# Optimization experiments

Hardware: AMD Instinct MI355X
Metric: run time of the kernel (lower is better)

## Reference

```python
import jax, jax.numpy as jnp
import numpy as np
from jax import lax

KERNEL = 15
IGNORE = 255


def setup_inputs() -> dict:
    key = jax.random.key(0)
    k1, k2 = jax.random.split(key)
    B, C, H, W = 32, 2, 480, 864
    logits = jax.random.normal(k1, (B, C, H, W), dtype=jnp.float32)
    labels = jax.random.randint(k2, (B, H, W), 0, 2, dtype=jnp.int32)
    return {"logits": logits, "labels": labels}


def _boundary_edgemap(labels):
    # labels: [B, H, W] int32 with values in {0, 1, IGNORE}
    lbl = labels.astype(jnp.int32)
    # np_label = label*255, with ignore pixels set to 0 (matches cv2 path)
    np_label = jnp.where(lbl == IGNORE, 0, lbl * 255)
    win = (1, KERNEL, KERNEL)
    strides = (1, 1, 1)
    # cv2.erode with ones kernel == 15x15 min filter (border value +inf -> pad 255)
    erosion = lax.reduce_window(np_label, jnp.int32(255), lax.min, win, strides, "SAME")
    # cv2.dilate == 15x15 max filter (border value -inf -> pad 0)
    dilation = lax.reduce_window(np_label, jnp.int32(0), lax.max, win, strides, "SAME")
    boundary = dilation - erosion  # >0 exactly on the morphological boundary band
    edgemap = jnp.where(boundary > 0, lbl, IGNORE)
    edgemap = jnp.where(lbl == IGNORE, IGNORE, edgemap)
    return edgemap


def reference(logits, labels):
    # logits: [B, C, H, W] log-probabilities, labels: [B, H, W]
    edgemap = _boundary_edgemap(labels)  # [B, H, W]
    valid = edgemap != IGNORE
    tgt = jnp.where(valid, edgemap, 0)  # safe index for ignored pixels
    # gather logits[b, tgt, h, w] -> [B, H, W]
    picked = jnp.take_along_axis(logits, tgt[:, None, :, :], axis=1)[:, 0]
    # NLLLoss with ignore_index: mean of -logp over valid pixels
    n_valid = jnp.maximum(jnp.sum(valid), 1)
    loss = -jnp.sum(jnp.where(valid, picked, 0.0)) / n_valid.astype(logits.dtype)
    return loss
```

## Files before the change

### kernel.cpp

```cpp
#include <hip/hip_runtime.h>


namespace {
constexpr int B_ = 32;
constexpr int H_ = 480;
constexpr int W_ = 864;
constexpr int HW = H_ * W_;
constexpr int R_ = 7;
constexpr int TH_ = 16;
constexpr int LH = TH_ + 2 * R_;
constexpr int SW = 216;
constexpr int NSX = W_ / SW;
constexpr int NSY = H_ / TH_;
constexpr int NBLK = B_ * NSX * NSY;
}

typedef unsigned long long u64;

__device__ __forceinline__ u64 shfl_up64(u64 x, int d) {
  return __shfl_up(x, d, 64);
}
__device__ __forceinline__ u64 shfl_dn64(u64 x, int d) {
  return __shfl_down(x, d, 64);
}

extern "C" __global__ __launch_bounds__(64, 2)
void boundary_loss_main(const float* __restrict__ logits,
                        const int* __restrict__ labels,
                        double2* __restrict__ partials)
{
  const int lane = threadIdx.x;
  const int bid = blockIdx.x;
  const int lb = (bid & 7) * (NBLK / 8) + (bid >> 3);
  const int img = lb / (NSX * NSY);
  const int r = lb - img * (NSX * NSY);
  const int strip = r / NSY;
  const int seg = r - strip * NSY;
  const int gr0 = seg * TH_;

  const int cb0 = strip * SW - 8 + 4 * lane;
  const bool colinb = (cb0 >= 0) && (cb0 + 3 < W_);
  const int cbc = colinb ? cb0 : (cb0 < 0 ? 0 : W_ - 4);
  const bool labok = colinb && (lane < 58);
  const bool outl = (lane >= 2) && (lane < 56);

  const int* __restrict__ lab = labels + img * HW + cbc;
  const float* __restrict__ lg = logits + (size_t)(2 * img) * HW;
  const float* pg = lg + (size_t)gr0 * W_ + cb0;

  u64 f0 = 0, f1 = 0, f2 = 0, f3 = 0;
  unsigned cp0 = 0, cp1 = 0, cp2 = 0, cp3 = 0;
#pragma unroll
  for (int a = 0; a < LH; ++a) {
    int gr = gr0 - R_ + a;
    gr = gr < 0 ? 0 : (gr >= H_ ? H_ - 1 : gr);
    const int4 v = *(const int4*)(lab + gr * W_);
    const unsigned e1x = (v.x == 1), e1y = (v.y == 1),
                   e1z = (v.z == 1), e1w = (v.w == 1);
    f0 |= (u64)(1u + e1x) << (2 * a);
    f1 |= (u64)(1u + e1y) << (2 * a);
    f2 |= (u64)(1u + e1z) << (2 * a);
    f3 |= (u64)(1u + e1w) << (2 * a);
    if (a >= R_ && a < R_ + TH_) {
      const int sh = 2 * (a - R_);
      cp0 |= (e1x | ((unsigned)(v.x == 255) << 1)) << sh;
      cp1 |= (e1y | ((unsigned)(v.y == 255) << 1)) << sh;
      cp2 |= (e1z | ((unsigned)(v.z == 255) << 1)) << sh;
      cp3 |= (e1w | ((unsigned)(v.w == 255) << 1)) << sh;
    }
  }
  {
    const int tv = gr0 == 0 ? R_ : 0;
    const int hi = LH < (H_ + R_ - gr0) ? LH : (H_ + R_ - gr0);
    u64 rm = (2 * (hi - tv) >= 32)
                 ? ((((1ull << (2 * (hi - tv) - 32)) - 1ull) << 32) | 0xFFFFFFFFull)
                 : ((1ull << (2 * (hi - tv))) - 1ull);
    rm <<= 2 * tv;
    if (!colinb) rm = 0;
    f0 &= rm; f1 &= rm; f2 &= rm; f3 &= rm;
  }

  float4 qa0[4], qa1[4], qb0[4], qb1[4];
#define ISSUE(G0, G1, q)                                                    \
  if (outl) {                                                               \
    const float* p_ = pg + (size_t)(4 * (q)) * W_;                          \
    _Pragma("unroll") for (int o = 0; o < 4; ++o) {                         \
      G0[o] = *(const float4*)(p_ + (size_t)o * W_);                        \
      G1[o] = *(const float4*)(p_ + (size_t)o * W_ + HW);                   \
    }                                                                       \
  }

  ISSUE(qa0, qa1, 0)

  const u64 allf = f0 | f1 | f2 | f3;
  const u64 s2 = f2 | f3, s3 = f1 | s2;
  const u64 p2 = f0 | f1, p3 = p2 | f2;
  const u64 core = shfl_up64(allf, 1) | allf | shfl_dn64(allf, 1);
  u64 w0 = core | shfl_up64(s3, 2);
  u64 w1 = core | shfl_up64(s2, 2) | shfl_dn64(f0, 2);
  u64 w2 = core | shfl_up64(f3, 2) | shfl_dn64(p2, 2);
  u64 w3 = core | shfl_dn64(p3, 2);

  w0 |= w0 >> 2;  w0 |= w0 >> 4;  w0 |= w0 >> 8;  w0 |= w0 >> 14;
  w1 |= w1 >> 2;  w1 |= w1 >> 4;  w1 |= w1 >> 8;  w1 |= w1 >> 14;
  w2 |= w2 >> 2;  w2 |= w2 >> 4;  w2 |= w2 >> 8;  w2 |= w2 >> 14;
  w3 |= w3 >> 2;  w3 |= w3 >> 4;  w3 |= w3 >> 8;  w3 |= w3 >> 14;

  double lsum = 0.0;
  unsigned lcnt = 0;
#define CONSUME(G0, G1, q)                                                  \
  if (outl) {                                                               \
    _Pragma("unroll") for (int o = 0; o < 4; ++o) {                         \
      const int ro = 4 * (q) + o;                                           \
      const unsigned b0 = (unsigned)(w0 >> (2 * ro)) & 3u;                  \
      const unsigned b1 = (unsigned)(w1 >> (2 * ro)) & 3u;                  \
      const unsigned b2 = (unsigned)(w2 >> (2 * ro)) & 3u;                  \
      const unsigned b3 = (unsigned)(w3 >> (2 * ro)) & 3u;                  \
      const unsigned q0 = (cp0 >> (2 * ro)) & 3u;                           \
      const unsigned q1 = (cp1 >> (2 * ro)) & 3u;                           \
      const unsigned q2 = (cp2 >> (2 * ro)) & 3u;                           \
      const unsigned q3 = (cp3 >> (2 * ro)) & 3u;                           \
      const float4 a = G0[o], c = G1[o];                                    \
      const bool k0 = (b0 == 3u) && !(q0 & 2u);                             \
      const bool k1 = (b1 == 3u) && !(q1 & 2u);                             \
      const bool k2 = (b2 == 3u) && !(q2 & 2u);                             \
      const bool k3 = (b3 == 3u) && !(q3 & 2u);                             \
      lsum += k0 ? (double)((q0 & 1u) ? c.x : a.x) : 0.0;                   \
      lsum += k1 ? (double)((q1 & 1u) ? c.y : a.y) : 0.0;                   \
      lsum += k2 ? (double)((q2 & 1u) ? c.z : a.z) : 0.0;                   \
      lsum += k3 ? (double)((q3 & 1u) ? c.w : a.w) : 0.0;                   \
      lcnt += (unsigned)k0 + k1 + k2 + k3;                                  \
    }                                                                       \
  }

  ISSUE(qb0, qb1, 1)
  CONSUME(qa0, qa1, 0)
  __builtin_amdgcn_sched_barrier(0);
  ISSUE(qa0, qa1, 2)
  CONSUME(qb0, qb1, 1)
  __builtin_amdgcn_sched_barrier(0);
  ISSUE(qb0, qb1, 3)
  CONSUME(qa0, qa1, 2)
  __builtin_amdgcn_sched_barrier(0);
  CONSUME(qb0, qb1, 3)
#undef ISSUE
#undef CONSUME

#pragma unroll
  for (int off = 32; off > 0; off >>= 1) {
    lsum += __shfl_down(lsum, off, 64);
    lcnt += __shfl_down(lcnt, off, 64);
  }
  if (lane == 0) partials[bid] = make_double2(lsum, (double)lcnt);
}

extern "C" __global__ __launch_bounds__(1024)
void boundary_loss_final(const double2* __restrict__ partials,
                         float* __restrict__ out)
{
  __shared__ double red_s[16];
  __shared__ double red_c[16];
  const int tid = threadIdx.x;
  double s = 0.0, c = 0.0;
  for (int i = tid; i < NBLK; i += 1024) {
    const double2 p = partials[i];
    s += p.x;
    c += p.y;
  }
#pragma unroll
  for (int off = 32; off > 0; off >>= 1) {
    s += __shfl_down(s, off, 64);
    c += __shfl_down(c, off, 64);
  }
  const int wave = tid >> 6;
  if ((tid & 63) == 0) { red_s[wave] = s; red_c[wave] = c; }
  __syncthreads();
  if (tid == 0) {
    double ts = 0.0, tc = 0.0;
#pragma unroll
    for (int i = 0; i < 16; ++i) { ts += red_s[i]; tc += red_c[i]; }
    if (tc < 1.0) tc = 1.0;
    out[0] = (float)(-ts / tc);
  }
}

extern "C" void kernel_launch(void* const* d_in, const int* in_sizes, int n_in,
                              void* d_out, int out_size, void* d_ws, size_t ws_size,
                              hipStream_t stream)
{
  const float* logits = (const float*)d_in[0];
  const int* labels = (const int*)d_in[1];
  float* out = (float*)d_out;
  double2* partials = (double2*)d_ws;

  boundary_loss_main<<<dim3(NBLK), 64, 0, stream>>>(logits, labels, partials);
  boundary_loss_final<<<1, 1024, 0, stream>>>(partials, out);
}
```

Measured before the change: 194.5 us.

## Split boundary loss into horizontal-dilation pre-pass with packed flags and logits pass

Adds a first kernel that reads each label row once, computes the horizontal 15-wide min/max window flags plus class/ignore bits, and packs them as 16-bit per 4-pixel groups into workspace. The second kernel reads these compact flags (including the vertical halo) instead of re-reading int32 labels with a 14-row halo, then does only the vertical reduction and the logits gather. This reduces redundant label traffic and halo overhead at the cost of an extra launch and a flag buffer write/read round trip. It falls back to the original fused kernel if the workspace is too small.

Result: slower. 200.5 us (+3.1%).

```diff
diff --git a/kernel.cpp b/kernel.cpp
--- a/kernel.cpp
+++ b/kernel.cpp
@@ -13,6 +13,12 @@
 constexpr int NSX = W_ / SW;
 constexpr int NSY = H_ / TH_;
 constexpr int NBLK = B_ * NSX * NSY;
+constexpr int X4 = W_ / 4;
+constexpr int RG = H_ / 16;
+constexpr int NB1 = B_ * RG;
+constexpr size_t FLAG_OFF = 61440;
+constexpr size_t FLAG_BYTES = (size_t)B_ * H_ * X4 * 2;
+constexpr size_t WS_NEED = FLAG_OFF + FLAG_BYTES;
 }
 
 typedef unsigned long long u64;
@@ -24,10 +30,72 @@
   return __shfl_down(x, d, 64);
 }
 
+extern "C" __global__ __launch_bounds__(256, 2)
+void boundary_pass1(const int* __restrict__ labels,
+                    unsigned short* __restrict__ flags)
+{
+  const int tid = threadIdx.x;
+  const int lane = tid & 63;
+  const int wv = tid >> 6;
+  const int lb = (blockIdx.x & 7) * (NB1 / 8) + (blockIdx.x >> 3);
+  const int img = lb / RG;
+  const int rg = lb - img * RG;
+  const int y0 = rg * 16;
+  const int strip = wv;
+
+  const int cb0 = strip * SW - 8 + 4 * lane;
+  const bool colinb = (cb0 >= 0) && (cb0 + 3 < W_);
+  const int cbc = colinb ? cb0 : (cb0 < 0 ? 0 : W_ - 4);
+  const bool labok = colinb && (lane < 58);
+  const bool outl = (lane >= 2) && (lane < 56);
+  const int* __restrict__ lab = labels + img * HW + cbc;
+
+  unsigned f0 = 0, f1 = 0, f2 = 0, f3 = 0;
+  unsigned c0 = 0, c1 = 0, c2 = 0, c3 = 0;
+#pragma unroll
+  for (int a = 0; a < 16; ++a) {
+    const int4 v = *(const int4*)(lab + (size_t)(y0 + a) * W_);
+    const unsigned m = labok ? 3u : 0u;
+    const int sh = 2 * a;
+    f0 |= (((v.x == 1) ? 2u : 1u) & m) << sh;
+    f1 |= (((v.y == 1) ? 2u : 1u) & m) << sh;
+    f2 |= (((v.z == 1) ? 2u : 1u) & m) << sh;
+    f3 |= (((v.w == 1) ? 2u : 1u) & m) << sh;
+    c0 |= (((v.x == 1) ? 1u : 0u) | ((v.x == 255) ? 2u : 0u)) << sh;
+    c1 |= (((v.y == 1) ? 1u : 0u) | ((v.y == 255) ? 2u : 0u)) << sh;
+    c2 |= (((v.z == 1) ? 1u : 0u) | ((v.z == 255) ? 2u : 0u)) << sh;
+    c3 |= (((v.w == 1) ? 1u : 0u) | ((v.w == 255) ? 2u : 0u)) << sh;
+  }
+
+  const unsigned allf = f0 | f1 | f2 | f3;
+  const unsigned s2 = f2 | f3, s3 = f1 | s2;
+  const unsigned p2 = f0 | f1, p3 = p2 | f2;
+  const unsigned core = __shfl_up(allf, 1, 64) | allf | __shfl_down(allf, 1, 64);
+  const unsigned w0 = core | __shfl_up(s3, 2, 64);
+  const unsigned w1 = core | __shfl_up(s2, 2, 64) | __shfl_down(f0, 2, 64);
+  const unsigned w2 = core | __shfl_up(f3, 2, 64) | __shfl_down(p2, 2, 64);
+  const unsigned w3 = core | __shfl_down(p3, 2, 64);
+
+  if (outl) {
+    unsigned short* fp =
+        flags + ((size_t)img * H_ + y0) * X4 + strip * 54 + (lane - 2);
+#pragma unroll
+    for (int a = 0; a < 16; ++a) {
+      const int sh = 2 * a;
+      const unsigned n0 = ((w0 >> sh) & 3u) | (((c0 >> sh) & 3u) << 2);
+      const unsigned n1 = ((w1 >> sh) & 3u) | (((c1 >> sh) & 3u) << 2);
+      const unsigned n2 = ((w2 >> sh) & 3u) | (((c2 >> sh) & 3u) << 2);
+      const unsigned n3 = ((w3 >> sh) & 3u) | (((c3 >> sh) & 3u) << 2);
+      fp[(size_t)a * X4] =
+          (unsigned short)(n0 | (n1 << 4) | (n2 << 8) | (n3 << 12));
+    }
+  }
+}
+
 extern "C" __global__ __launch_bounds__(64, 2)
-void boundary_loss_main(const float* __restrict__ logits,
-                        const int* __restrict__ labels,
-                        double2* __restrict__ partials)
+void boundary_pass2(const float* __restrict__ logits,
+                    const unsigned short* __restrict__ flags,
+                    double2* __restrict__ partials)
 {
   const int lane = threadIdx.x;
   const int bid = blockIdx.x;
@@ -39,6 +107,119 @@
   const int gr0 = seg * TH_;
 
   const int cb0 = strip * SW - 8 + 4 * lane;
+  const bool outl = (lane >= 2) && (lane < 56);
+  const float* __restrict__ lg = logits + (size_t)(2 * img) * HW;
+  const float* pg = lg + (size_t)gr0 * W_ + cb0;
+
+  u64 f0 = 0, f1 = 0, f2 = 0, f3 = 0;
+  unsigned cp0 = 0, cp1 = 0, cp2 = 0, cp3 = 0;
+  if (outl) {
+    const unsigned short* fp =
+        flags + (size_t)img * H_ * X4 + strip * 54 + (lane - 2);
+#pragma unroll
+    for (int a = 0; a < LH; ++a) {
+      int gr = gr0 - R_ + a;
+      gr = gr < 0 ? 0 : (gr >= H_ ? H_ - 1 : gr);
+      const unsigned t = fp[(size_t)gr * X4];
+      f0 |= (u64)(t & 3u) << (2 * a);
+      f1 |= (u64)((t >> 4) & 3u) << (2 * a);
+      f2 |= (u64)((t >> 8) & 3u) << (2 * a);
+      f3 |= (u64)((t >> 12) & 3u) << (2 * a);
+      if (a >= R_ && a < R_ + TH_) {
+        const int sh = 2 * (a - R_);
+        cp0 |= ((t >> 2) & 3u) << sh;
+        cp1 |= ((t >> 6) & 3u) << sh;
+        cp2 |= ((t >> 10) & 3u) << sh;
+        cp3 |= ((t >> 14) & 3u) << sh;
+      }
+    }
+    const int tv = gr0 == 0 ? R_ : 0;
+    const int hi = LH < (H_ + R_ - gr0) ? LH : (H_ + R_ - gr0);
+    u64 rm = (2 * (hi - tv) >= 32)
+                 ? ((((1ull << (2 * (hi - tv) - 32)) - 1ull) << 32) | 0xFFFFFFFFull)
+                 : ((1ull << (2 * (hi - tv))) - 1ull);
+    rm <<= 2 * tv;
+    f0 &= rm; f1 &= rm; f2 &= rm; f3 &= rm;
+  }
+
+  float4 qa0[4], qa1[4], qb0[4], qb1[4];
+#define ISSUE(G0, G1, q)                                                    \
+  if (outl) {                                                               \
+    const float* p_ = pg + (size_t)(4 * (q)) * W_;                          \
+    _Pragma("unroll") for (int o = 0; o < 4; ++o) {                         \
+      G0[o] = *(const float4*)(p_ + (size_t)o * W_);                        \
+      G1[o] = *(const float4*)(p_ + (size_t)o * W_ + HW);                   \
+    }                                                                       \
+  }
+  ISSUE(qa0, qa1, 0)
+
+  f0 |= f0 >> 2;  f0 |= f0 >> 4;  f0 |= f0 >> 8;  f0 |= f0 >> 14;
+  f1 |= f1 >> 2;  f1 |= f1 >> 4;  f1 |= f1 >> 8;  f1 |= f1 >> 14;
+  f2 |= f2 >> 2;  f2 |= f2 >> 4;  f2 |= f2 >> 8;  f2 |= f2 >> 14;
+  f3 |= f3 >> 2;  f3 |= f3 >> 4;  f3 |= f3 >> 8;  f3 |= f3 >> 14;
+
+  double lsum = 0.0;
+  unsigned lcnt = 0;
+#define CONSUME(G0, G1, q)                                                  \
+  if (outl) {                                                               \
+    _Pragma("unroll") for (int o = 0; o < 4; ++o) {                         \
+      const int ro = 4 * (q) + o;                                           \
+      const unsigned b0 = (unsigned)(f0 >> (2 * ro)) & 3u;                  \
+      const unsigned b1 = (unsigned)(f1 >> (2 * ro)) & 3u;                  \
+      const unsigned b2 = (unsigned)(f2 >> (2 * ro)) & 3u;                  \
+      const unsigned b3 = (unsigned)(f3 >> (2 * ro)) & 3u;                  \
+      const unsigned q0 = (cp0 >> (2 * ro)) & 3u;                           \
+      const unsigned q1 = (cp1 >> (2 * ro)) & 3u;                           \
+      const unsigned q2 = (cp2 >> (2 * ro)) & 3u;                           \
+      const unsigned q3 = (cp3 >> (2 * ro)) & 3u;                           \
+      const float4 a = G0[o], c = G1[o];                                    \
+      const bool k0 = (b0 == 3u) && !(q0 & 2u);                             \
+      const bool k1 = (b1 == 3u) && !(q1 & 2u);                             \
+      const bool k2 = (b2 == 3u) && !(q2 & 2u);                             \
+      const bool k3 = (b3 == 3u) && !(q3 & 2u);                             \
+      lsum += k0 ? (double)((q0 & 1u) ? c.x : a.x) : 0.0;                   \
+      lsum += k1 ? (double)((q1 & 1u) ? c.y : a.y) : 0.0;                   \
+      lsum += k2 ? (double)((q2 & 1u) ? c.z : a.z) : 0.0;                   \
+      lsum += k3 ? (double)((q3 & 1u) ? c.w : a.w) : 0.0;                   \
+      lcnt += (unsigned)k0 + k1 + k2 + k3;                                  \
+    }                                                                       \
+  }
+  ISSUE(qb0, qb1, 1)
+  CONSUME(qa0, qa1, 0)
+  __builtin_amdgcn_sched_barrier(0);
+  ISSUE(qa0, qa1, 2)
+  CONSUME(qb0, qb1, 1)
+  __builtin_amdgcn_sched_barrier(0);
+  ISSUE(qb0, qb1, 3)
+  CONSUME(qa0, qa1, 2)
+  __builtin_amdgcn_sched_barrier(0);
+  CONSUME(qb0, qb1, 3)
+#undef ISSUE
+#undef CONSUME
+
+#pragma unroll
+  for (int off = 32; off > 0; off >>= 1) {
+    lsum += __shfl_down(lsum, off, 64);
+    lcnt += __shfl_down(lcnt, off, 64);
+  }
+  if (lane == 0) partials[bid] = make_double2(lsum, (double)lcnt);
+}
+
+extern "C" __global__ __launch_bounds__(64, 2)
+void boundary_loss_mono(const float* __restrict__ logits,
+                        const int* __restrict__ labels,
+                        double2* __restrict__ partials)
+{
+  const int lane = threadIdx.x;
+  const int bid = blockIdx.x;
+  const int lb = (bid & 7) * (NBLK / 8) + (bid >> 3);
+  const int img = lb / (NSX * NSY);
+  const int r = lb - img * (NSX * NSY);
+  const int strip = r / NSY;
+  const int seg = r - strip * NSY;
+  const int gr0 = seg * TH_;
+
+  const int cb0 = strip * SW - 8 + 4 * lane;
   const bool colinb = (cb0 >= 0) && (cb0 + 3 < W_);
   const int cbc = colinb ? cb0 : (cb0 < 0 ? 0 : W_ - 4);
   const bool labok = colinb && (lane < 58);
@@ -57,10 +238,11 @@
     const int4 v = *(const int4*)(lab + gr * W_);
     const unsigned e1x = (v.x == 1), e1y = (v.y == 1),
                    e1z = (v.z == 1), e1w = (v.w == 1);
-    f0 |= (u64)(1u + e1x) << (2 * a);
-    f1 |= (u64)(1u + e1y) << (2 * a);
-    f2 |= (u64)(1u + e1z) << (2 * a);
-    f3 |= (u64)(1u + e1w) << (2 * a);
+    const unsigned m = labok ? 3u : 0u;
+    f0 |= (u64)((1u + e1x) & m) << (2 * a);
+    f1 |= (u64)((1u + e1y) & m) << (2 * a);
+    f2 |= (u64)((1u + e1z) & m) << (2 * a);
+    f3 |= (u64)((1u + e1w) & m) << (2 * a);
     if (a >= R_ && a < R_ + TH_) {
       const int sh = 2 * (a - R_);
       cp0 |= (e1x | ((unsigned)(v.x == 255) << 1)) << sh;
@@ -89,7 +271,6 @@
       G1[o] = *(const float4*)(p_ + (size_t)o * W_ + HW);                   \
     }                                                                       \
   }
-
   ISSUE(qa0, qa1, 0)
 
   const u64 allf = f0 | f1 | f2 | f3;
@@ -100,7 +281,6 @@
   u64 w1 = core | shfl_up64(s2, 2) | shfl_dn64(f0, 2);
   u64 w2 = core | shfl_up64(f3, 2) | shfl_dn64(p2, 2);
   u64 w3 = core | shfl_dn64(p3, 2);
-
   w0 |= w0 >> 2;  w0 |= w0 >> 4;  w0 |= w0 >> 8;  w0 |= w0 >> 14;
   w1 |= w1 >> 2;  w1 |= w1 >> 4;  w1 |= w1 >> 8;  w1 |= w1 >> 14;
   w2 |= w2 >> 2;  w2 |= w2 >> 4;  w2 |= w2 >> 8;  w2 |= w2 >> 14;
@@ -132,7 +312,6 @@
       lcnt += (unsigned)k0 + k1 + k2 + k3;                                  \
     }                                                                       \
   }
-
   ISSUE(qb0, qb1, 1)
   CONSUME(qa0, qa1, 0)
   __builtin_amdgcn_sched_barrier(0);
@@ -193,6 +372,12 @@
   float* out = (float*)d_out;
   double2* partials = (double2*)d_ws;
 
-  boundary_loss_main<<<dim3(NBLK), 64, 0, stream>>>(logits, labels, partials);
+  if (ws_size >= WS_NEED) {
+    unsigned short* flags = (unsigned short*)((char*)d_ws + FLAG_OFF);
+    boundary_pass1<<<dim3(NB1), 256, 0, stream>>>(labels, flags);
+    boundary_pass2<<<dim3(NBLK), 64, 0, stream>>>(logits, flags, partials);
+  } else {
+    boundary_loss_mono<<<dim3(NBLK), 64, 0, stream>>>(logits, labels, partials);
+  }
   boundary_loss_final<<<1, 1024, 0, stream>>>(partials, out);
 }
```
